# Performance work log

Hardware: AMD Instinct MI355X
Metric: run time of the kernel (lower is better)

## Reference

```python
import jax, jax.numpy as jnp
import numpy as np
from jax import lax

B, C, H, W = 4, 256, 64, 64
R1, R2 = 4, 8


def conv1x1(x, w, b):
    # x: [B,C,H,W], w: [O,C], b: [O]
    return jnp.einsum('bchw,oc->bohw', x, w) + b[None, :, None, None]


def dwconv3x3(x, w, b):
    # depthwise 3x3, SAME padding. w: [C,1,3,3]
    y = lax.conv_general_dilated(x, w, window_strides=(1, 1), padding='SAME',
                                 dimension_numbers=('NCHW', 'OIHW', 'NCHW'),
                                 feature_group_count=x.shape[1])
    return y + b[None, :, None, None]


def setup_inputs() -> dict:
    key = jax.random.key(0)
    ks = jax.random.split(key, 20)
    s = 0.02
    inp = {
        'x':   jax.random.normal(ks[0], (B, C, H, W), jnp.float32),
        'Wq':  jax.random.normal(ks[1], (C, C), jnp.float32) * s,
        'bq':  jnp.zeros((C,), jnp.float32),
        'Wk':  jax.random.normal(ks[2], (C, 1, 3, 3), jnp.float32) * s,
        'bk':  jnp.zeros((C,), jnp.float32),
        'Wv':  jax.random.normal(ks[3], (C, 1, 3, 3), jnp.float32) * s,
        'bv':  jnp.zeros((C,), jnp.float32),
        'Wl':  jax.random.normal(ks[4], (C, 1, 3, 3), jnp.float32) * s,
        'bl':  jnp.zeros((C,), jnp.float32),
        'Ws1': jax.random.normal(ks[5], (C // R1, C), jnp.float32) * s,
        'bs1': jnp.zeros((C // R1,), jnp.float32),
        'Ws2': jax.random.normal(ks[6], (C, C // R1), jnp.float32) * s,
        'bs2': jnp.zeros((C,), jnp.float32),
        'Wc1': jax.random.normal(ks[7], (C // R2, C), jnp.float32) * s,
        'bc1': jnp.zeros((C // R2,), jnp.float32),
        'Wc2': jax.random.normal(ks[8], (C, C // R2), jnp.float32) * s,
        'bc2': jnp.zeros((C,), jnp.float32),
        'Wo':  jax.random.normal(ks[9], (C, C), jnp.float32) * s,
        'bo':  jnp.zeros((C,), jnp.float32),
    }
    return inp


def reference(x, Wq, bq, Wk, bk, Wv, bv, Wl, bl, Ws1, bs1, Ws2, bs2,
              Wc1, bc1, Wc2, bc2, Wo, bo):
    b_, c_, h_, w_ = x.shape
    hw = h_ * w_
    scale = jnp.sqrt(jnp.float32(c_))

    q = conv1x1(x, Wq, bq).reshape(b_, c_, hw).transpose(0, 2, 1)   # [B,HW,C]
    k = dwconv3x3(x, Wk, bk).reshape(b_, c_, hw)                    # [B,C,HW]
    v_img = dwconv3x3(x, Wv, bv)                                    # [B,C,H,W]
    v = v_img.reshape(b_, c_, hw).transpose(0, 2, 1)                # [B,HW,C]

    attn = jax.nn.softmax(jnp.einsum('bnc,bcm->bnm', q, k) / scale, axis=-1)
    global_out = jnp.einsum('bnm,bmc->bnc', attn, v)                # [B,HW,C]
    global_out = global_out.transpose(0, 2, 1).reshape(b_, c_, h_, w_)

    local_out = dwconv3x3(v_img, Wl, bl)                            # [B,C,H,W]

    spatial_weight = jax.nn.sigmoid(
        conv1x1(jax.nn.relu(conv1x1(local_out, Ws1, bs1)), Ws2, bs2))

    gap = jnp.mean(global_out, axis=(2, 3), keepdims=True)          # [B,C,1,1]
    channel_weight = jax.nn.sigmoid(
        conv1x1(jax.nn.relu(conv1x1(gap, Wc1, bc1)), Wc2, bc2))     # [B,C,1,1]

    fused = global_out * channel_weight + local_out * spatial_weight
    return conv1x1(fused, Wo, bo) + x
```

## Files before the change

### kernel.cpp

```cpp
#include <hip/hip_runtime.h>
#include <hip/hip_fp8.h>
#include <stdint.h>

typedef unsigned short u16;
typedef unsigned char u8;
typedef __attribute__((ext_vector_type(8))) __bf16 bf16x8;
typedef __attribute__((ext_vector_type(8))) short short8s;
typedef __attribute__((ext_vector_type(4))) float float4v;
typedef __attribute__((ext_vector_type(16))) float floatx16;

static constexpr int NB = 4, NC = 256, NH = 64, NW = 64, NHW = 4096;
static constexpr int BC = 32;
static constexpr int NKV = 4;
static constexpr int KVCHUNK = NHW / NKV;

static constexpr size_t MB = 1ull << 20;
static constexpr size_t OFF_KBF    = 0;
static constexpr size_t OFF_LBF    = 8 * MB;
static constexpr size_t OFF_GT     = 0;
static constexpr size_t OFF_XT     = 16 * MB;
static constexpr size_t OFF_FUSEDT = 16 * MB;
static constexpr size_t OFF_QT8    = 24 * MB;
static constexpr size_t OFF_KT8    = 32 * MB;
static constexpr size_t OFF_VBF    = 40 * MB;
static constexpr size_t OFF_LT     = 48 * MB;
static constexpr size_t OFF_OPART  = 56 * MB;
static constexpr size_t OFF_LPART  = 88 * MB;
static constexpr size_t OFF_HIDT   = OFF_LPART + 256 * 1024;
static constexpr size_t OFF_GAP    = OFF_HIDT + 2 * MB;
static constexpr size_t OFF_WQB    = OFF_GAP + 8 * 1024;
static constexpr size_t OFF_WS1B   = OFF_WQB + 131072;
static constexpr size_t OFF_WS2B   = OFF_WS1B + 32768;
static constexpr size_t OFF_WOB    = OFF_WS2B + 32768;

__device__ __forceinline__ float b2f(u16 h) {
    union { float f; unsigned u; } v; v.u = ((unsigned)h) << 16; return v.f;
}
__device__ __forceinline__ u16 f2b(float f) {
    union { float f; unsigned u; } v; v.f = f;
    unsigned r = v.u + 0x7fffu + ((v.u >> 16) & 1u);
    return (u16)(r >> 16);
}
__device__ __forceinline__ u8 f2f8(float f) {
    __hip_fp8_e4m3 h(f);
    return *reinterpret_cast<u8*>(&h);
}

__device__ __forceinline__ void load_lds16(const void* gsrc, void* ldst) {
    __builtin_amdgcn_global_load_lds(
        (__attribute__((address_space(1))) void*)(uintptr_t)gsrc,
        (__attribute__((address_space(3))) void*)ldst,
        16, 0, 0);
}

__global__ __launch_bounds__(256) void prep(
    const float* __restrict__ x,
    const float* __restrict__ Wq, const float* __restrict__ Ws1,
    const float* __restrict__ Ws2, const float* __restrict__ Wo,
    const float* __restrict__ Wk, const float* __restrict__ bk,
    const float* __restrict__ Wv, const float* __restrict__ bv,
    const float* __restrict__ Wl, const float* __restrict__ bl,
    u16* __restrict__ Wqb, u16* __restrict__ Ws1b, u16* __restrict__ Ws2b, u16* __restrict__ Wob,
    float* __restrict__ gap,
    u16* __restrict__ k_bf, u16* __restrict__ vN, u16* __restrict__ local_bf,
    u16* __restrict__ xT)
{
    __shared__ __align__(16) unsigned char pshm[9216];
    const int bid = blockIdx.x;
    const int t = threadIdx.x;

    if (bid < 644) {
        int id = bid * 256 + t;
        if (id < 65536)        Wqb[id] = f2b(Wq[id]);
        else if (id < 81920)   Ws1b[id - 65536] = f2b(Ws1[id - 65536]);
        else if (id < 98304)   Ws2b[id - 81920] = f2b(Ws2[id - 81920]);
        else if (id < 163840)  Wob[id - 98304] = f2b(Wo[id - 98304]);
        else if (id < 164864)  gap[id - 163840] = 0.f;
        return;
    }
    if (bid < 2692) {
        int l = bid - 644;
        int xx0 = t & 63, cl = t >> 6;
        int y0 = (l & 7) * 8;
        int c  = ((l >> 3) & 63) * 4 + cl;
        int b  = l >> 9;
        const float* xb = x + ((size_t)b * NC + c) * NHW;
        float wk[9], wv[9], wl[9];
#pragma unroll
        for (int i = 0; i < 9; i++) { wk[i] = Wk[c*9+i]; wv[i] = Wv[c*9+i]; wl[i] = Wl[c*9+i]; }
        float bkc = bk[c], bvc = bv[c], blc = bl[c];

        auto ldx = [&](int y) -> float {
            return ((unsigned)y <= 63u) ? xb[y * 64 + xx0] : 0.f;
        };
        auto conv3 = [&](const float* w9, float a, float bm, float cc) -> float {
            float au = __shfl_up(a, 1, 64),   ad = __shfl_down(a, 1, 64);
            float bu = __shfl_up(bm, 1, 64),  bd = __shfl_down(bm, 1, 64);
            float cu = __shfl_up(cc, 1, 64),  cd = __shfl_down(cc, 1, 64);
            float al = (xx0 == 0) ? 0.f : au, ar = (xx0 == 63) ? 0.f : ad;
            float bl_ = (xx0 == 0) ? 0.f : bu, br = (xx0 == 63) ? 0.f : bd;
            float cle = (xx0 == 0) ? 0.f : cu, cr = (xx0 == 63) ? 0.f : cd;
            return w9[0]*al + w9[1]*a  + w9[2]*ar
                 + w9[3]*bl_ + w9[4]*bm + w9[5]*br
                 + w9[6]*cle + w9[7]*cc + w9[8]*cr;
        };

        float xm2 = ldx(y0 - 2), xm1 = ldx(y0 - 1), x0v = ldx(y0), xp1 = ldx(y0 + 1);
        float vm1 = (y0 - 1 >= 0) ? (bvc + conv3(wv, xm2, xm1, x0v)) : 0.f;
        float v0  = bvc + conv3(wv, xm1, x0v, xp1);

        size_t base = ((size_t)b * NC + c) * NHW;
#pragma unroll
        for (int yi = 0; yi < 8; yi++) {
            int y = y0 + yi;
            float xp2 = ldx(y + 2);
            float vp1 = (y + 1 <= 63) ? (bvc + conv3(wv, x0v, xp1, xp2)) : 0.f;
            float kk  = bkc + conv3(wk, xm1, x0v, xp1);
            float ll  = blc + conv3(wl, vm1, v0, vp1);
            size_t o = base + y * 64 + xx0;
            k_bf[o]     = f2b(kk);
            vN[o]       = f2b(v0);
            local_bf[o] = f2b(ll);
            xm1 = x0v; x0v = xp1; xp1 = xp2;
            vm1 = v0;  v0 = vp1;
        }
        return;
    }
    {
        u16 (*tile)[72] = reinterpret_cast<u16 (*)[72]>(pshm);
        int l = bid - 2692;
        int n0 = (l & 63) * 64;
        int c0 = ((l >> 6) & 3) * 64;
        int b  = l >> 8;
        const float* src = x + (size_t)b * NC * NHW;
        u16* dst = xT + (size_t)b * NHW * NC;
        int c = t >> 2, nb = (t & 3) * 16;
#pragma unroll
        for (int q = 0; q < 4; q++) {
            float4 v = *(const float4*)(src + (size_t)(c0 + c) * NHW + n0 + nb + q * 4);
            tile[c][nb + q * 4 + 0] = f2b(v.x);
            tile[c][nb + q * 4 + 1] = f2b(v.y);
            tile[c][nb + q * 4 + 2] = f2b(v.z);
            tile[c][nb + q * 4 + 3] = f2b(v.w);
        }
        __syncthreads();
        int cl = t & 63, ng = t >> 6;
#pragma unroll
        for (int j = 0; j < 16; j++) {
            int n = ng * 16 + j;
            dst[(size_t)(n0 + n) * NC + c0 + cl] = tile[cl][n];
        }
    }
}

__global__ __launch_bounds__(256) void transpose_bf(
    const u16* __restrict__ k_bf, const u16* __restrict__ local_bf,
    u8* __restrict__ kT8, u16* __restrict__ localT)
{
    __shared__ u16 tile[64][72];
    int n0 = blockIdx.x * 64, c0 = blockIdx.y * 64;
    int zb = blockIdx.z, b = zb >> 1;
    const u16* src = (zb & 1) ? local_bf : k_bf;
    src += (size_t)b * NC * NHW;
    int t = threadIdx.x;
    int c = t >> 2, nb = (t & 3) * 16;
    *(short8s*)&tile[c][nb]     = *(const short8s*)(src + (size_t)(c0 + c) * NHW + n0 + nb);
    *(short8s*)&tile[c][nb + 8] = *(const short8s*)(src + (size_t)(c0 + c) * NHW + n0 + nb + 8);
    __syncthreads();
    int cl = t & 63, ng = t >> 6;
    if (zb & 1) {
        u16* dst = localT + (size_t)b * NHW * NC;
#pragma unroll
        for (int j = 0; j < 16; j++) {
            int n = ng * 16 + j;
            dst[(size_t)(n0 + n) * NC + c0 + cl] = tile[cl][n];
        }
    } else {
        u8* dst = kT8 + (size_t)b * NHW * NC;
#pragma unroll
        for (int j = 0; j < 16; j++) {
            int n = ng * 16 + j;
            dst[(size_t)(n0 + n) * NC + c0 + cl] = f2f8(b2f(tile[cl][n]));
        }
    }
}

__global__ __launch_bounds__(256) void gemm_qhid(
    const u16* __restrict__ xT, const u16* __restrict__ Wqb, const float* __restrict__ bq,
    u8* __restrict__ qT8,
    const u16* __restrict__ localT, const u16* __restrict__ Ws1b, const float* __restrict__ bs1,
    u16* __restrict__ hidT)
{
    const int t = threadIdx.x, w = t >> 6, lane = t & 63;
    const int lm = lane & 15, quad = lane >> 4;
    const int zone = blockIdx.x >> 9;
    const int l = blockIdx.x & 511;
    const int b = l >> 7;
    const int s_base = (l & 127) * 32 + (w & 1) * 16;

    if (zone == 0) {
        const int ch = (w >> 1) * 128;
        const u16* xTb = xT + (size_t)b * NHW * NC;
        u8* qTb = qT8 + (size_t)b * NHW * NC;
        bf16x8 aq[8];
#pragma unroll
        for (int kt = 0; kt < 8; kt++)
            aq[kt] = *(const bf16x8*)(xTb + (size_t)(s_base + lm) * NC + kt * 32 + quad * 8);
        float4v acc[8];
#pragma unroll
        for (int j = 0; j < 8; j++) acc[j] = (float4v){0.f, 0.f, 0.f, 0.f};
#pragma unroll
        for (int kt = 0; kt < 8; kt++) {
#pragma unroll
            for (int j = 0; j < 8; j++) {
                bf16x8 bw = *(const bf16x8*)(Wqb + (size_t)(ch + j * 16 + lm) * 256 + kt * 32 + quad * 8);
                acc[j] = __builtin_amdgcn_mfma_f32_16x16x32_bf16(aq[kt], bw, acc[j], 0, 0, 0);
            }
        }
#pragma unroll
        for (int j = 0; j < 8; j++) {
            int cout = ch + j * 16 + lm;
            float bb = bq[cout];
#pragma unroll
            for (int r = 0; r < 4; r++) {
                int s = s_base + quad * 4 + r;
                qTb[(size_t)s * NC + cout] = f2f8(acc[j][r] + bb);
            }
        }
    } else {
        const int ch = (w >> 1) * 32;
        const u16* lTb = localT + (size_t)b * NHW * NC;
        u16* hTb = hidT + (size_t)b * NHW * 64;
        bf16x8 aq[8];
#pragma unroll
        for (int kt = 0; kt < 8; kt++)
            aq[kt] = *(const bf16x8*)(lTb + (size_t)(s_base + lm) * NC + kt * 32 + quad * 8);
        float4v acc[2];
#pragma unroll
        for (int j = 0; j < 2; j++) acc[j] = (float4v){0.f, 0.f, 0.f, 0.f};
#pragma unroll
        for (int kt = 0; kt < 8; kt++) {
#pragma unroll
            for (int j = 0; j < 2; j++) {
                bf16x8 bw = *(const bf16x8*)(Ws1b + (size_t)(ch + j * 16 + lm) * 256 + kt * 32 + quad * 8);
                acc[j] = __builtin_amdgcn_mfma_f32_16x16x32_bf16(aq[kt], bw, acc[j], 0, 0, 0);
            }
        }
#pragma unroll
        for (int j = 0; j < 2; j++) {
            int h = ch + j * 16 + lm;
            float bb = bs1[h];
#pragma unroll
            for (int r = 0; r < 4; r++) {
                int s = s_base + quad * 4 + r;
                hTb[(size_t)s * 64 + h] = f2b(fmaxf(acc[j][r] + bb, 0.0f));
            }
        }
    }
}

__device__ __forceinline__ void stage_tiles(
    const u8* __restrict__ kb, const u16* __restrict__ vNb, int kv0,
    u8* KlB, u16* VlB, int w, int lane)
{
#pragma unroll
    for (int i = 0; i < 2; i++) {
        int g = (w * 2 + i) * 64 + lane;
        int n = g >> 4, jj = g & 15, cc = jj ^ (n & 15);
        load_lds16(kb + (size_t)(kv0 + n) * NC + cc * 16, KlB + (w * 2 + i) * 1024);
    }
#pragma unroll
    for (int i = 0; i < 4; i++) {
        int g = (w * 4 + i) * 64 + lane;
        int c = g >> 2, jj = g & 3, ck = (jj - (c >> 1)) & 3;
        load_lds16(vNb + (size_t)c * NHW + kv0 + ck * 8, (char*)VlB + (w * 4 + i) * 1024);
    }
}

__global__ __launch_bounds__(256, 2) void attn_split(
    const u8* __restrict__ qT8, const u8* __restrict__ kT8,
    const u16* __restrict__ vN, u16* __restrict__ Opart, float* __restrict__ lpart)
{
    __shared__ __align__(16) u8 Kl[2][BC * 256];
    __shared__ __align__(16) u16 Vl[2][256 * BC];

    const int combo = blockIdx.x & 15;
    const int b  = combo >> 2;
    const int jc = combo & 3;
    const int n0 = (blockIdx.x >> 4) * 128;
    const int t = threadIdx.x;
    const int w = t >> 6, lane = t & 63;
    const int lr = lane & 31, l5 = lane >> 5;

    const u8* qb = qT8 + (size_t)b * NHW * NC;
    const u8* kb = kT8 + (size_t)b * NHW * NC;
    const u16* vNb = vN + (size_t)b * NC * NHW;

    long aq[16];
    {
        int qrow = n0 + w * 32 + lr;
#pragma unroll
        for (int kt = 0; kt < 16; kt++)
            aq[kt] = *(const long*)(qb + (size_t)qrow * NC + kt * 16 + l5 * 8);
    }

    floatx16 oacc[8];
#pragma unroll
    for (int i = 0; i < 8; i++)
#pragma unroll
        for (int j = 0; j < 16; j++) oacc[i][j] = 0.f;
    float lsum = 0.f;

    const int kvbeg = jc * KVCHUNK;
    stage_tiles(kb, vNb, kvbeg, Kl[0], Vl[0], w, lane);

    int buf = 0;
#pragma unroll 1
    for (int it = 0; it < KVCHUNK / BC; it++) {
        const int kv0 = kvbeg + it * BC;
        const int nxt = (it + 1 < KVCHUNK / BC) ? (kv0 + BC) : kvbeg;
        stage_tiles(kb, vNb, nxt, Kl[buf ^ 1], Vl[buf ^ 1], w, lane);
        asm volatile("s_waitcnt vmcnt(6)" ::: "memory");
        __builtin_amdgcn_s_barrier();

        const u8* KlB = Kl[buf];
        const u16* VlB = Vl[buf];

        floatx16 sacc;
#pragma unroll
        for (int j = 0; j < 16; j++) sacc[j] = 0.f;
#pragma unroll
        for (int kt = 0; kt < 16; kt++) {
            long ak = *(const long*)&KlB[lr * 256 + ((kt ^ (lr & 15)) * 16) + l5 * 8];
            sacc = __builtin_amdgcn_mfma_f32_32x32x16_fp8_fp8(ak, aq[kt], sacc, 0, 0, 0);
        }
        unsigned pk[8];
#pragma unroll
        for (int g2 = 0; g2 < 8; g2++) {
            float p0 = __expf(sacc[g2 * 2 + 0] * 0.0625f);
            float p1 = __expf(sacc[g2 * 2 + 1] * 0.0625f);
            lsum += p0 + p1;
            union { float f; unsigned u; } a, bb;
            a.f = p0; bb.f = p1;
            pk[g2] = (bb.u & 0xffff0000u) | (a.u >> 16);
        }
        unsigned rA = (unsigned)__shfl_xor((int)(l5 ? pk[0] : pk[2]), 32, 64);
        unsigned rB = (unsigned)__shfl_xor((int)(l5 ? pk[1] : pk[3]), 32, 64);
        unsigned rC = (unsigned)__shfl_xor((int)(l5 ? pk[4] : pk[6]), 32, 64);
        unsigned rD = (unsigned)__shfl_xor((int)(l5 ? pk[5] : pk[7]), 32, 64);
        union { unsigned u[4]; bf16x8 v; } f0, f1;
        f0.u[0] = l5 ? rA : pk[0];  f0.u[1] = l5 ? rB : pk[1];
        f0.u[2] = l5 ? pk[2] : rA;  f0.u[3] = l5 ? pk[3] : rB;
        f1.u[0] = l5 ? rC : pk[4];  f1.u[1] = l5 ? rD : pk[5];
        f1.u[2] = l5 ? pk[6] : rC;  f1.u[3] = l5 ? pk[7] : rD;

#pragma unroll
        for (int ct = 0; ct < 8; ct++) {
            int c = ct * 32 + lr;
            int vb = c * 32;
            bf16x8 bv0 = *(const bf16x8*)&VlB[vb + (((l5 + (c >> 1)) & 3)) * 8];
            bf16x8 bv1 = *(const bf16x8*)&VlB[vb + (((2 + l5 + (c >> 1)) & 3)) * 8];
            oacc[ct] = __builtin_amdgcn_mfma_f32_32x32x16_bf16(f0.v, bv0, oacc[ct], 0, 0, 0);
            oacc[ct] = __builtin_amdgcn_mfma_f32_32x32x16_bf16(f1.v, bv1, oacc[ct], 0, 0, 0);
        }
        __builtin_amdgcn_s_barrier();
        buf ^= 1;
    }

    lsum += __shfl_xor(lsum, 32, 64);
    u16* Ob = Opart + ((size_t)(b * NKV + jc) * NHW + n0 + w * 32) * NC;
#pragma unroll
    for (int reg = 0; reg < 16; reg++) {
        int row = (reg & 3) + 8 * (reg >> 2) + 4 * l5;
#pragma unroll
        for (int ct = 0; ct < 8; ct++)
            Ob[(size_t)row * NC + ct * 32 + lr] = f2b(oacc[ct][reg]);
    }
    if (lane < 32)
        lpart[(size_t)(b * NKV + jc) * NHW + n0 + w * 32 + lr] = lsum;
}

__global__ __launch_bounds__(256) void attn_combine(
    const u16* __restrict__ Opart, const float* __restrict__ lpart,
    u16* __restrict__ gT, float* __restrict__ gap)
{
    __shared__ float gsum[256];
    int t = threadIdx.x;
    gsum[t] = 0.f;
    __syncthreads();
    int b = blockIdx.y;
    int n = blockIdx.x * 8 + (t >> 5);
    int c0 = (t & 31) * 8;
    float acc[8] = {};
    float l = 0.f;
#pragma unroll
    for (int j = 0; j < NKV; j++) {
        const u16* op = Opart + ((size_t)(b * NKV + j) * NHW + n) * NC + c0;
        short8s v = *(const short8s*)op;
#pragma unroll
        for (int i = 0; i < 8; i++) acc[i] += b2f(((const u16*)&v)[i]);
        l += lpart[(size_t)(b * NKV + j) * NHW + n];
    }
    float inv = 1.0f / l;
#pragma unroll
    for (int i = 0; i < 8; i++) acc[i] *= inv;
    short8s vo;
#pragma unroll
    for (int i = 0; i < 8; i++) ((u16*)&vo)[i] = f2b(acc[i]);
    *(short8s*)(gT + ((size_t)b * NHW + n) * NC + c0) = vo;
#pragma unroll
    for (int i = 0; i < 8; i++) atomicAdd(&gsum[c0 + i], acc[i]);
    __syncthreads();
    atomicAdd(&gap[b * NC + t], gsum[t]);
}

__global__ __launch_bounds__(256) void gemm_swfused_mfma(
    const u16* __restrict__ hidT, const u16* __restrict__ Ws2b, const float* __restrict__ bs2,
    const u16* __restrict__ gT, const u16* __restrict__ localT,
    const float* __restrict__ gap,
    const float* __restrict__ Wc1, const float* __restrict__ bc1,
    const float* __restrict__ Wc2, const float* __restrict__ bc2,
    u16* __restrict__ fusedT)
{
    __shared__ float g[256], h1[32], cwl[256];
    __shared__ float ph[32][9];
    const int t = threadIdx.x, w = t >> 6, lane = t & 63;
    const int lm = lane & 15, quad = lane >> 4;
    const int b = blockIdx.y;

    g[t] = gap[b * 256 + t] * (1.0f / 4096.0f);
    __syncthreads();
    {
        int h = t & 31, part = t >> 5;
        float s = 0.f;
        for (int c = part * 32; c < part * 32 + 32; c++) s += Wc1[h * 256 + c] * g[c];
        ph[h][part] = s;
    }
    __syncthreads();
    if (t < 32) {
        float s = bc1[t];
#pragma unroll
        for (int p = 0; p < 8; p++) s += ph[t][p];
        h1[t] = fmaxf(s, 0.f);
    }
    __syncthreads();
    {
        float s = bc2[t];
#pragma unroll
        for (int j = 0; j < 32; j++) s += Wc2[t * 32 + j] * h1[j];
        cwl[t] = 1.0f / (1.0f + __expf(-s));
    }
    __syncthreads();

    const int s_base = blockIdx.x * 32 + (w & 1) * 16;
    const int ch = (w >> 1) * 128;
    const u16* hTb = hidT + (size_t)b * NHW * 64;
    const u16* lTb = localT + (size_t)b * NHW * NC;
    const u16* gTb = gT + (size_t)b * NHW * NC;
    u16* fTb = fusedT + (size_t)b * NHW * NC;

    bf16x8 aq[2];
#pragma unroll
    for (int kt = 0; kt < 2; kt++)
        aq[kt] = *(const bf16x8*)(hTb + (size_t)(s_base + lm) * 64 + kt * 32 + quad * 8);

    float4v acc[8];
#pragma unroll
    for (int j = 0; j < 8; j++) acc[j] = (float4v){0.f, 0.f, 0.f, 0.f};

#pragma unroll
    for (int kt = 0; kt < 2; kt++) {
#pragma unroll
        for (int j = 0; j < 8; j++) {
            bf16x8 bw = *(const bf16x8*)(Ws2b + (size_t)(ch + j * 16 + lm) * 64 + kt * 32 + quad * 8);
            acc[j] = __builtin_amdgcn_mfma_f32_16x16x32_bf16(aq[kt], bw, acc[j], 0, 0, 0);
        }
    }
#pragma unroll
    for (int j = 0; j < 8; j++) {
        int c = ch + j * 16 + lm;
        float bb = bs2[c];
        float cwv = cwl[c];
#pragma unroll
        for (int r = 0; r < 4; r++) {
            int s = s_base + quad * 4 + r;
            float sw = 1.0f / (1.0f + __expf(-(acc[j][r] + bb)));
            float gg = b2f(gTb[(size_t)s * NC + c]);
            float lo = b2f(lTb[(size_t)s * NC + c]);
            fTb[(size_t)s * NC + c] = f2b(gg * cwv + lo * sw);
        }
    }
}

__global__ __launch_bounds__(256) void gemm_out_mfma(
    const u16* __restrict__ Wob, const u16* __restrict__ fusedT, const float* __restrict__ bo,
    const float* __restrict__ x, float* __restrict__ out)
{
    const int t = threadIdx.x, w = t >> 6, lane = t & 63;
    const int lm = lane & 15, quad = lane >> 4;
    const int b = blockIdx.z;
    const int o_base = blockIdx.x * 32 + (w & 1) * 16;
    const int n_base = blockIdx.y * 256 + (w >> 1) * 128;
    const u16* fTb = fusedT + (size_t)b * NHW * NC;

    bf16x8 aw[8];
#pragma unroll
    for (int kt = 0; kt < 8; kt++)
        aw[kt] = *(const bf16x8*)(Wob + (size_t)(o_base + lm) * 256 + kt * 32 + quad * 8);

    float4v acc[8];
#pragma unroll
    for (int j = 0; j < 8; j++) acc[j] = (float4v){0.f, 0.f, 0.f, 0.f};

#pragma unroll
    for (int kt = 0; kt < 8; kt++) {
#pragma unroll
        for (int j = 0; j < 8; j++) {
            bf16x8 bf = *(const bf16x8*)(fTb + (size_t)(n_base + j * 16 + lm) * NC + kt * 32 + quad * 8);
            acc[j] = __builtin_amdgcn_mfma_f32_16x16x32_bf16(aw[kt], bf, acc[j], 0, 0, 0);
        }
    }
#pragma unroll
    for (int r = 0; r < 4; r++) {
        int o = o_base + quad * 4 + r;
        float bb = bo[o];
        size_t rowoff = ((size_t)b * NC + o) * NHW;
#pragma unroll
        for (int j = 0; j < 8; j++) {
            int n = n_base + j * 16 + lm;
            out[rowoff + n] = acc[j][r] + bb + x[rowoff + n];
        }
    }
}

extern "C" void kernel_launch(void* const* d_in, const int* in_sizes, int n_in,
                              void* d_out, int out_size, void* d_ws, size_t ws_size,
                              hipStream_t stream)
{
    const float* x   = (const float*)d_in[0];
    const float* Wq  = (const float*)d_in[1];
    const float* bq  = (const float*)d_in[2];
    const float* Wk  = (const float*)d_in[3];
    const float* bk  = (const float*)d_in[4];
    const float* Wv  = (const float*)d_in[5];
    const float* bv  = (const float*)d_in[6];
    const float* Wl  = (const float*)d_in[7];
    const float* bl  = (const float*)d_in[8];
    const float* Ws1 = (const float*)d_in[9];
    const float* bs1 = (const float*)d_in[10];
    const float* Ws2 = (const float*)d_in[11];
    const float* bs2 = (const float*)d_in[12];
    const float* Wc1 = (const float*)d_in[13];
    const float* bc1 = (const float*)d_in[14];
    const float* Wc2 = (const float*)d_in[15];
    const float* bc2 = (const float*)d_in[16];
    const float* Wo  = (const float*)d_in[17];
    const float* bo  = (const float*)d_in[18];
    float* out = (float*)d_out;

    char* ws = (char*)d_ws;
    u16* k_bf     = (u16*)(ws + OFF_KBF);
    u16* local_bf = (u16*)(ws + OFF_LBF);
    u16* gT       = (u16*)(ws + OFF_GT);
    u16* xT       = (u16*)(ws + OFF_XT);
    u16* fusedT   = (u16*)(ws + OFF_FUSEDT);
    u8*  qT8      = (u8*)(ws + OFF_QT8);
    u8*  kT8      = (u8*)(ws + OFF_KT8);
    u16* vN       = (u16*)(ws + OFF_VBF);
    u16* localT   = (u16*)(ws + OFF_LT);
    u16* Opart    = (u16*)(ws + OFF_OPART);
    float* lpart  = (float*)(ws + OFF_LPART);
    u16* hidT     = (u16*)(ws + OFF_HIDT);
    float* gap    = (float*)(ws + OFF_GAP);
    u16* Wqb      = (u16*)(ws + OFF_WQB);
    u16* Ws1b     = (u16*)(ws + OFF_WS1B);
    u16* Ws2b     = (u16*)(ws + OFF_WS2B);
    u16* Wob      = (u16*)(ws + OFF_WOB);

    prep<<<dim3(3716), 256, 0, stream>>>(x, Wq, Ws1, Ws2, Wo, Wk, bk, Wv, bv, Wl, bl,
                                         Wqb, Ws1b, Ws2b, Wob, gap, k_bf, vN, local_bf, xT);
    transpose_bf<<<dim3(64, 4, 8), 256, 0, stream>>>(k_bf, local_bf, kT8, localT);
    gemm_qhid<<<dim3(1024), 256, 0, stream>>>(xT, Wqb, bq, qT8, localT, Ws1b, bs1, hidT);
    attn_split<<<dim3(512), 256, 0, stream>>>(qT8, kT8, vN, Opart, lpart);
    attn_combine<<<dim3(NHW / 8, 4), 256, 0, stream>>>(Opart, lpart, gT, gap);
    gemm_swfused_mfma<<<dim3(128, 4), 256, 0, stream>>>(hidT, Ws2b, bs2, gT, localT,
                                                        gap, Wc1, bc1, Wc2, bc2, fusedT);
    gemm_out_mfma<<<dim3(8, 16, 4), 256, 0, stream>>>(Wob, fusedT, bo, x, out);
}
```

Before: 279.7 us.

## Use fp8 for V, P and partial outputs in attention; merge kernels

V is now stored as fp8 and the P·V product uses fp8 MFMA. Softmax probabilities are packed with cvt_pk_fp8 and exchanged via permlane32_swap instead of shuffles. Partial outputs are written as fp8, which halves Opart traffic and V staging bytes. The transpose and Q-GEMM kernels are merged into one launch, and the hidden-GEMM is folded into the attention launch as extra blocks. The cost is lower precision in the attention value path and partial sums.

```diff
diff --git a/kernel.cpp b/kernel.cpp
--- a/kernel.cpp
+++ b/kernel.cpp
@@ -22,7 +22,7 @@
 static constexpr size_t OFF_FUSEDT = 16 * MB;
 static constexpr size_t OFF_QT8    = 24 * MB;
 static constexpr size_t OFF_KT8    = 32 * MB;
-static constexpr size_t OFF_VBF    = 40 * MB;
+static constexpr size_t OFF_V8     = 40 * MB;
 static constexpr size_t OFF_LT     = 48 * MB;
 static constexpr size_t OFF_OPART  = 56 * MB;
 static constexpr size_t OFF_LPART  = 88 * MB;
@@ -62,7 +62,7 @@
     const float* __restrict__ Wl, const float* __restrict__ bl,
     u16* __restrict__ Wqb, u16* __restrict__ Ws1b, u16* __restrict__ Ws2b, u16* __restrict__ Wob,
     float* __restrict__ gap,
-    u16* __restrict__ k_bf, u16* __restrict__ vN, u16* __restrict__ local_bf,
+    u16* __restrict__ k_bf, u8* __restrict__ vN8, u16* __restrict__ local_bf,
     u16* __restrict__ xT)
 {
     __shared__ __align__(16) unsigned char pshm[9216];
@@ -119,7 +119,7 @@
             float ll  = blc + conv3(wl, vm1, v0, vp1);
             size_t o = base + y * 64 + xx0;
             k_bf[o]     = f2b(kk);
-            vN[o]       = f2b(v0);
+            vN8[o]      = f2f8(v0);
             local_bf[o] = f2b(ll);
             xm1 = x0v; x0v = xp1; xp1 = xp2;
             vm1 = v0;  v0 = vp1;
@@ -153,52 +153,48 @@
     }
 }
 
-__global__ __launch_bounds__(256) void transpose_bf(
+__global__ __launch_bounds__(256) void mid(
     const u16* __restrict__ k_bf, const u16* __restrict__ local_bf,
-    u8* __restrict__ kT8, u16* __restrict__ localT)
-{
-    __shared__ u16 tile[64][72];
-    int n0 = blockIdx.x * 64, c0 = blockIdx.y * 64;
-    int zb = blockIdx.z, b = zb >> 1;
-    const u16* src = (zb & 1) ? local_bf : k_bf;
-    src += (size_t)b * NC * NHW;
-    int t = threadIdx.x;
-    int c = t >> 2, nb = (t & 3) * 16;
-    *(short8s*)&tile[c][nb]     = *(const short8s*)(src + (size_t)(c0 + c) * NHW + n0 + nb);
-    *(short8s*)&tile[c][nb + 8] = *(const short8s*)(src + (size_t)(c0 + c) * NHW + n0 + nb + 8);
-    __syncthreads();
-    int cl = t & 63, ng = t >> 6;
-    if (zb & 1) {
-        u16* dst = localT + (size_t)b * NHW * NC;
-#pragma unroll
-        for (int j = 0; j < 16; j++) {
-            int n = ng * 16 + j;
-            dst[(size_t)(n0 + n) * NC + c0 + cl] = tile[cl][n];
-        }
-    } else {
-        u8* dst = kT8 + (size_t)b * NHW * NC;
-#pragma unroll
-        for (int j = 0; j < 16; j++) {
-            int n = ng * 16 + j;
-            dst[(size_t)(n0 + n) * NC + c0 + cl] = f2f8(b2f(tile[cl][n]));
-        }
-    }
-}
-
-__global__ __launch_bounds__(256) void gemm_qhid(
+    u8* __restrict__ kT8, u16* __restrict__ localT,
     const u16* __restrict__ xT, const u16* __restrict__ Wqb, const float* __restrict__ bq,
-    u8* __restrict__ qT8,
-    const u16* __restrict__ localT, const u16* __restrict__ Ws1b, const float* __restrict__ bs1,
-    u16* __restrict__ hidT)
-{
-    const int t = threadIdx.x, w = t >> 6, lane = t & 63;
-    const int lm = lane & 15, quad = lane >> 4;
-    const int zone = blockIdx.x >> 9;
-    const int l = blockIdx.x & 511;
-    const int b = l >> 7;
-    const int s_base = (l & 127) * 32 + (w & 1) * 16;
-
-    if (zone == 0) {
+    u8* __restrict__ qT8)
+{
+    __shared__ __align__(16) u16 tile[64][72];
+    const int t = threadIdx.x;
+    const int bid = blockIdx.x;
+    if (bid < 2048) {
+        int n0 = (bid & 63) * 64, c0 = ((bid >> 6) & 3) * 64;
+        int zb = bid >> 8, b = zb >> 1;
+        const u16* src = (zb & 1) ? local_bf : k_bf;
+        src += (size_t)b * NC * NHW;
+        int c = t >> 2, nb = (t & 3) * 16;
+        *(short8s*)&tile[c][nb]     = *(const short8s*)(src + (size_t)(c0 + c) * NHW + n0 + nb);
+        *(short8s*)&tile[c][nb + 8] = *(const short8s*)(src + (size_t)(c0 + c) * NHW + n0 + nb + 8);
+        __syncthreads();
+        int cl = t & 63, ng = t >> 6;
+        if (zb & 1) {
+            u16* dst = localT + (size_t)b * NHW * NC;
+#pragma unroll
+            for (int j = 0; j < 16; j++) {
+                int n = ng * 16 + j;
+                dst[(size_t)(n0 + n) * NC + c0 + cl] = tile[cl][n];
+            }
+        } else {
+            u8* dst = kT8 + (size_t)b * NHW * NC;
+#pragma unroll
+            for (int j = 0; j < 16; j++) {
+                int n = ng * 16 + j;
+                dst[(size_t)(n0 + n) * NC + c0 + cl] = f2f8(b2f(tile[cl][n]));
+            }
+        }
+        return;
+    }
+    {
+        const int w = t >> 6, lane = t & 63;
+        const int lm = lane & 15, quad = lane >> 4;
+        const int l = bid - 2048;
+        const int b = l >> 7;
+        const int s_base = (l & 127) * 32 + (w & 1) * 16;
         const int ch = (w >> 1) * 128;
         const u16* xTb = xT + (size_t)b * NHW * NC;
         u8* qTb = qT8 + (size_t)b * NHW * NC;
@@ -227,14 +223,51 @@
                 qTb[(size_t)s * NC + cout] = f2f8(acc[j][r] + bb);
             }
         }
-    } else {
+    }
+}
+
+__device__ __forceinline__ void stage_tiles(
+    const u8* __restrict__ kb, const u8* __restrict__ vb8, int kv0,
+    u8* KlB, u8* VlB, int w, int lane)
+{
+#pragma unroll
+    for (int i = 0; i < 2; i++) {
+        int g = (w * 2 + i) * 64 + lane;
+        int n = g >> 4, jj = g & 15, cc = jj ^ (n & 15);
+        load_lds16(kb + (size_t)(kv0 + n) * NC + cc * 16, KlB + (w * 2 + i) * 1024);
+    }
+#pragma unroll
+    for (int i = 0; i < 2; i++) {
+        int g = (w * 2 + i) * 64 + lane;
+        int c = g >> 1, h = g & 1, e = (c >> 2) & 1;
+        load_lds16(vb8 + (size_t)c * NHW + kv0 + (h ^ e) * 16, VlB + (w * 2 + i) * 1024);
+    }
+}
+
+__global__ __launch_bounds__(256, 2) void attn_hid(
+    const u8* __restrict__ qT8, const u8* __restrict__ kT8,
+    const u8* __restrict__ vN8, u8* __restrict__ Opart8, float* __restrict__ lpart,
+    const u16* __restrict__ localT, const u16* __restrict__ Ws1b, const float* __restrict__ bs1,
+    u16* __restrict__ hidT)
+{
+    __shared__ __align__(16) u8 Kl[2][BC * 256];
+    __shared__ __align__(16) u8 Vl[2][256 * BC];
+
+    const int t = threadIdx.x;
+    const int w = t >> 6, lane = t & 63;
+
+    if (blockIdx.x >= 512) {
+        const int lm = lane & 15, quad = lane >> 4;
+        const int l = blockIdx.x - 512;
+        const int b = l >> 7;
+        const int s_base = (l & 127) * 32 + (w & 1) * 16;
         const int ch = (w >> 1) * 32;
         const u16* lTb = localT + (size_t)b * NHW * NC;
         u16* hTb = hidT + (size_t)b * NHW * 64;
-        bf16x8 aq[8];
+        bf16x8 ah[8];
 #pragma unroll
         for (int kt = 0; kt < 8; kt++)
-            aq[kt] = *(const bf16x8*)(lTb + (size_t)(s_base + lm) * NC + kt * 32 + quad * 8);
+            ah[kt] = *(const bf16x8*)(lTb + (size_t)(s_base + lm) * NC + kt * 32 + quad * 8);
         float4v acc[2];
 #pragma unroll
         for (int j = 0; j < 2; j++) acc[j] = (float4v){0.f, 0.f, 0.f, 0.f};
@@ -243,7 +276,7 @@
 #pragma unroll
             for (int j = 0; j < 2; j++) {
                 bf16x8 bw = *(const bf16x8*)(Ws1b + (size_t)(ch + j * 16 + lm) * 256 + kt * 32 + quad * 8);
-                acc[j] = __builtin_amdgcn_mfma_f32_16x16x32_bf16(aq[kt], bw, acc[j], 0, 0, 0);
+                acc[j] = __builtin_amdgcn_mfma_f32_16x16x32_bf16(ah[kt], bw, acc[j], 0, 0, 0);
             }
         }
 #pragma unroll
@@ -256,45 +289,18 @@
                 hTb[(size_t)s * 64 + h] = f2b(fmaxf(acc[j][r] + bb, 0.0f));
             }
         }
-    }
-}
-
-__device__ __forceinline__ void stage_tiles(
-    const u8* __restrict__ kb, const u16* __restrict__ vNb, int kv0,
-    u8* KlB, u16* VlB, int w, int lane)
-{
-#pragma unroll
-    for (int i = 0; i < 2; i++) {
-        int g = (w * 2 + i) * 64 + lane;
-        int n = g >> 4, jj = g & 15, cc = jj ^ (n & 15);
-        load_lds16(kb + (size_t)(kv0 + n) * NC + cc * 16, KlB + (w * 2 + i) * 1024);
-    }
-#pragma unroll
-    for (int i = 0; i < 4; i++) {
-        int g = (w * 4 + i) * 64 + lane;
-        int c = g >> 2, jj = g & 3, ck = (jj - (c >> 1)) & 3;
-        load_lds16(vNb + (size_t)c * NHW + kv0 + ck * 8, (char*)VlB + (w * 4 + i) * 1024);
-    }
-}
-
-__global__ __launch_bounds__(256, 2) void attn_split(
-    const u8* __restrict__ qT8, const u8* __restrict__ kT8,
-    const u16* __restrict__ vN, u16* __restrict__ Opart, float* __restrict__ lpart)
-{
-    __shared__ __align__(16) u8 Kl[2][BC * 256];
-    __shared__ __align__(16) u16 Vl[2][256 * BC];
+        return;
+    }
 
     const int combo = blockIdx.x & 15;
     const int b  = combo >> 2;
     const int jc = combo & 3;
     const int n0 = (blockIdx.x >> 4) * 128;
-    const int t = threadIdx.x;
-    const int w = t >> 6, lane = t & 63;
     const int lr = lane & 31, l5 = lane >> 5;
 
     const u8* qb = qT8 + (size_t)b * NHW * NC;
     const u8* kb = kT8 + (size_t)b * NHW * NC;
-    const u16* vNb = vN + (size_t)b * NC * NHW;
+    const u8* vb8 = vN8 + (size_t)b * NC * NHW;
 
     long aq[16];
     {
@@ -312,19 +318,19 @@
     float lsum = 0.f;
 
     const int kvbeg = jc * KVCHUNK;
-    stage_tiles(kb, vNb, kvbeg, Kl[0], Vl[0], w, lane);
+    stage_tiles(kb, vb8, kvbeg, Kl[0], Vl[0], w, lane);
 
     int buf = 0;
 #pragma unroll 1
     for (int it = 0; it < KVCHUNK / BC; it++) {
         const int kv0 = kvbeg + it * BC;
         const int nxt = (it + 1 < KVCHUNK / BC) ? (kv0 + BC) : kvbeg;
-        stage_tiles(kb, vNb, nxt, Kl[buf ^ 1], Vl[buf ^ 1], w, lane);
-        asm volatile("s_waitcnt vmcnt(6)" ::: "memory");
+        stage_tiles(kb, vb8, nxt, Kl[buf ^ 1], Vl[buf ^ 1], w, lane);
+        asm volatile("s_waitcnt vmcnt(4)" ::: "memory");
         __builtin_amdgcn_s_barrier();
 
         const u8* KlB = Kl[buf];
-        const u16* VlB = Vl[buf];
+        const u8* VlB = Vl[buf];
 
         floatx16 sacc;
 #pragma unroll
@@ -334,54 +340,56 @@
             long ak = *(const long*)&KlB[lr * 256 + ((kt ^ (lr & 15)) * 16) + l5 * 8];
             sacc = __builtin_amdgcn_mfma_f32_32x32x16_fp8_fp8(ak, aq[kt], sacc, 0, 0, 0);
         }
-        unsigned pk[8];
-#pragma unroll
-        for (int g2 = 0; g2 < 8; g2++) {
-            float p0 = __expf(sacc[g2 * 2 + 0] * 0.0625f);
-            float p1 = __expf(sacc[g2 * 2 + 1] * 0.0625f);
-            lsum += p0 + p1;
-            union { float f; unsigned u; } a, bb;
-            a.f = p0; bb.f = p1;
-            pk[g2] = (bb.u & 0xffff0000u) | (a.u >> 16);
-        }
-        unsigned rA = (unsigned)__shfl_xor((int)(l5 ? pk[0] : pk[2]), 32, 64);
-        unsigned rB = (unsigned)__shfl_xor((int)(l5 ? pk[1] : pk[3]), 32, 64);
-        unsigned rC = (unsigned)__shfl_xor((int)(l5 ? pk[4] : pk[6]), 32, 64);
-        unsigned rD = (unsigned)__shfl_xor((int)(l5 ? pk[5] : pk[7]), 32, 64);
-        union { unsigned u[4]; bf16x8 v; } f0, f1;
-        f0.u[0] = l5 ? rA : pk[0];  f0.u[1] = l5 ? rB : pk[1];
-        f0.u[2] = l5 ? pk[2] : rA;  f0.u[3] = l5 ? pk[3] : rB;
-        f1.u[0] = l5 ? rC : pk[4];  f1.u[1] = l5 ? rD : pk[5];
-        f1.u[2] = l5 ? pk[6] : rC;  f1.u[3] = l5 ? pk[7] : rD;
+        unsigned u0 = 0, u1 = 0, u2 = 0, u3 = 0;
+        {
+            float p[16];
+#pragma unroll
+            for (int r = 0; r < 16; r++) {
+                p[r] = __expf(sacc[r] * 0.0625f);
+                lsum += p[r];
+            }
+            u0 = __builtin_amdgcn_cvt_pk_fp8_f32(p[0], p[1], 0, false);
+            u0 = __builtin_amdgcn_cvt_pk_fp8_f32(p[2], p[3], u0, true);
+            u1 = __builtin_amdgcn_cvt_pk_fp8_f32(p[4], p[5], 0, false);
+            u1 = __builtin_amdgcn_cvt_pk_fp8_f32(p[6], p[7], u1, true);
+            u2 = __builtin_amdgcn_cvt_pk_fp8_f32(p[8], p[9], 0, false);
+            u2 = __builtin_amdgcn_cvt_pk_fp8_f32(p[10], p[11], u2, true);
+            u3 = __builtin_amdgcn_cvt_pk_fp8_f32(p[12], p[13], 0, false);
+            u3 = __builtin_amdgcn_cvt_pk_fp8_f32(p[14], p[15], u3, true);
+        }
+        asm volatile("v_permlane32_swap_b32 %0, %1" : "+v"(u0), "+v"(u1));
+        asm volatile("v_permlane32_swap_b32 %0, %1" : "+v"(u2), "+v"(u3));
+        long A1 = (long)(((unsigned long long)u1 << 32) | u0);
+        long A2 = (long)(((unsigned long long)u3 << 32) | u2);
 
 #pragma unroll
         for (int ct = 0; ct < 8; ct++) {
             int c = ct * 32 + lr;
-            int vb = c * 32;
-            bf16x8 bv0 = *(const bf16x8*)&VlB[vb + (((l5 + (c >> 1)) & 3)) * 8];
-            bf16x8 bv1 = *(const bf16x8*)&VlB[vb + (((2 + l5 + (c >> 1)) & 3)) * 8];
-            oacc[ct] = __builtin_amdgcn_mfma_f32_32x32x16_bf16(f0.v, bv0, oacc[ct], 0, 0, 0);
-            oacc[ct] = __builtin_amdgcn_mfma_f32_32x32x16_bf16(f1.v, bv1, oacc[ct], 0, 0, 0);
+            int e2 = ((c >> 2) & 1) << 1;
+            long bv0 = *(const long*)&VlB[c * 32 + (l5 ^ e2) * 8];
+            long bv1 = *(const long*)&VlB[c * 32 + ((l5 ^ 2 ^ e2)) * 8];
+            oacc[ct] = __builtin_amdgcn_mfma_f32_32x32x16_fp8_fp8(A1, bv0, oacc[ct], 0, 0, 0);
+            oacc[ct] = __builtin_amdgcn_mfma_f32_32x32x16_fp8_fp8(A2, bv1, oacc[ct], 0, 0, 0);
         }
         __builtin_amdgcn_s_barrier();
         buf ^= 1;
     }
 
     lsum += __shfl_xor(lsum, 32, 64);
-    u16* Ob = Opart + ((size_t)(b * NKV + jc) * NHW + n0 + w * 32) * NC;
+    u8* Ob = Opart8 + ((size_t)(b * NKV + jc) * NHW + n0 + w * 32) * NC;
 #pragma unroll
     for (int reg = 0; reg < 16; reg++) {
         int row = (reg & 3) + 8 * (reg >> 2) + 4 * l5;
 #pragma unroll
         for (int ct = 0; ct < 8; ct++)
-            Ob[(size_t)row * NC + ct * 32 + lr] = f2b(oacc[ct][reg]);
+            Ob[(size_t)row * NC + ct * 32 + lr] = f2f8(oacc[ct][reg]);
     }
     if (lane < 32)
         lpart[(size_t)(b * NKV + jc) * NHW + n0 + w * 32 + lr] = lsum;
 }
 
 __global__ __launch_bounds__(256) void attn_combine(
-    const u16* __restrict__ Opart, const float* __restrict__ lpart,
+    const u8* __restrict__ Opart8, const float* __restrict__ lpart,
     u16* __restrict__ gT, float* __restrict__ gap)
 {
     __shared__ float gsum[256];
@@ -395,10 +403,17 @@
     float l = 0.f;
 #pragma unroll
     for (int j = 0; j < NKV; j++) {
-        const u16* op = Opart + ((size_t)(b * NKV + j) * NHW + n) * NC + c0;
-        short8s v = *(const short8s*)op;
-#pragma unroll
-        for (int i = 0; i < 8; i++) acc[i] += b2f(((const u16*)&v)[i]);
+        const u8* op = Opart8 + ((size_t)(b * NKV + j) * NHW + n) * NC + c0;
+        unsigned long long v = *(const unsigned long long*)op;
+        unsigned lo = (unsigned)v, hi = (unsigned)(v >> 32);
+        acc[0] += __builtin_amdgcn_cvt_f32_fp8(lo, 0);
+        acc[1] += __builtin_amdgcn_cvt_f32_fp8(lo, 1);
+        acc[2] += __builtin_amdgcn_cvt_f32_fp8(lo, 2);
+        acc[3] += __builtin_amdgcn_cvt_f32_fp8(lo, 3);
+        acc[4] += __builtin_amdgcn_cvt_f32_fp8(hi, 0);
+        acc[5] += __builtin_amdgcn_cvt_f32_fp8(hi, 1);
+        acc[6] += __builtin_amdgcn_cvt_f32_fp8(hi, 2);
+        acc[7] += __builtin_amdgcn_cvt_f32_fp8(hi, 3);
         l += lpart[(size_t)(b * NKV + j) * NHW + n];
     }
     float inv = 1.0f / l;
@@ -566,9 +581,9 @@
     u16* fusedT   = (u16*)(ws + OFF_FUSEDT);
     u8*  qT8      = (u8*)(ws + OFF_QT8);
     u8*  kT8      = (u8*)(ws + OFF_KT8);
-    u16* vN       = (u16*)(ws + OFF_VBF);
+    u8*  vN8      = (u8*)(ws + OFF_V8);
     u16* localT   = (u16*)(ws + OFF_LT);
-    u16* Opart    = (u16*)(ws + OFF_OPART);
+    u8*  Opart8   = (u8*)(ws + OFF_OPART);
     float* lpart  = (float*)(ws + OFF_LPART);
     u16* hidT     = (u16*)(ws + OFF_HIDT);
     float* gap    = (float*)(ws + OFF_GAP);
@@ -578,11 +593,11 @@
     u16* Wob      = (u16*)(ws + OFF_WOB);
 
     prep<<<dim3(3716), 256, 0, stream>>>(x, Wq, Ws1, Ws2, Wo, Wk, bk, Wv, bv, Wl, bl,
-                                         Wqb, Ws1b, Ws2b, Wob, gap, k_bf, vN, local_bf, xT);
-    transpose_bf<<<dim3(64, 4, 8), 256, 0, stream>>>(k_bf, local_bf, kT8, localT);
-    gemm_qhid<<<dim3(1024), 256, 0, stream>>>(xT, Wqb, bq, qT8, localT, Ws1b, bs1, hidT);
-    attn_split<<<dim3(512), 256, 0, stream>>>(qT8, kT8, vN, Opart, lpart);
-    attn_combine<<<dim3(NHW / 8, 4), 256, 0, stream>>>(Opart, lpart, gT, gap);
+                                         Wqb, Ws1b, Ws2b, Wob, gap, k_bf, vN8, local_bf, xT);
+    mid<<<dim3(2560), 256, 0, stream>>>(k_bf, local_bf, kT8, localT, xT, Wqb, bq, qT8);
+    attn_hid<<<dim3(1024), 256, 0, stream>>>(qT8, kT8, vN8, Opart8, lpart,
+                                             localT, Ws1b, bs1, hidT);
+    attn_combine<<<dim3(NHW / 8, 4), 256, 0, stream>>>(Opart8, lpart, gT, gap);
     gemm_swfused_mfma<<<dim3(128, 4), 256, 0, stream>>>(hidT, Ws2b, bs2, gT, localT,
                                                         gap, Wc1, bc1, Wc2, bc2, fusedT);
     gemm_out_mfma<<<dim3(8, 16, 4), 256, 0, stream>>>(Wob, fusedT, bo, x, out);
```

After: 279.1 us. No clear change (-0.2%).
